# Performance work log

Hardware: AMD Instinct MI355X
Metric: run time of the kernel (lower is better)

The kernel has to match this reference:

```python
import jax, jax.numpy as jnp
import numpy as np

D = 64      # hidden_dim
H = 4       # num_attention_heads
DH = D // H # head_dim
B = 64      # graphs per batch
SCALE = np.float32(np.sqrt(DH))


def _sage(x, edge, wl, bl, wr):
    # SAGEConv: lin_l(mean_j x_j) + lin_r(x_i); mean over incoming edges (dst = edge[1])
    src, dst = edge[0], edge[1]
    n = x.shape[0]
    agg = jax.ops.segment_sum(x[src], dst, num_segments=n)
    cnt = jax.ops.segment_sum(jnp.ones((edge.shape[1],), x.dtype), dst, num_segments=n)
    mean = agg / jnp.maximum(cnt, 1.0)[:, None]
    return mean @ wl + bl + x @ wr


def _cross_attn(xq, xk, w, b):
    # w: [3, D, D] stacked (Q, K, V) projections; b: [3, D]
    Q = (xq @ w[0] + b[0]).reshape(-1, H, DH)  # [Nq, H, DH]
    K = (xk @ w[1] + b[1]).reshape(-1, H, DH)  # [Nk, H, DH]
    V = (xk @ w[2] + b[2]).reshape(-1, H, DH)
    scores = jnp.einsum('qhd,khd->hqk', Q, K) / SCALE  # [H, Nq, Nk]
    wgt = jax.nn.softmax(scores, axis=-1)
    out = jnp.einsum('hqk,khd->qhd', wgt, V)
    return out.reshape(xq.shape[0], D)


def _segment_mean(x, seg, num):
    s = jax.ops.segment_sum(x, seg, num_segments=num)
    c = jax.ops.segment_sum(jnp.ones((x.shape[0],), x.dtype), seg, num_segments=num)
    return s / jnp.maximum(c, 1.0)[:, None]


def setup_inputs() -> dict:
    key = jax.random.key(0)
    ks = jax.random.split(key, 32)
    N_MOL, N_PROT, E_MOL, E_PROT = 2048, 8192, 32768, 131072
    MOL_IN, PROT_IN = 32, 64

    def lin(k, i, o, s=None):
        s = 1.0 / np.sqrt(i) if s is None else s
        return (jax.random.normal(k, (i, o), jnp.float32) * s)

    inp = {
        'x_mol': jax.random.normal(ks[0], (N_MOL, MOL_IN), jnp.float32),
        'x_prot': jax.random.normal(ks[1], (N_PROT, PROT_IN), jnp.float32),
        'm1_wl': lin(ks[2], MOL_IN, D), 'm1_bl': jnp.zeros((D,), jnp.float32), 'm1_wr': lin(ks[3], MOL_IN, D),
        'm2_wl': lin(ks[4], D, D), 'm2_bl': jnp.zeros((D,), jnp.float32), 'm2_wr': lin(ks[5], D, D),
        'p1_wl': lin(ks[6], PROT_IN, D), 'p1_bl': jnp.zeros((D,), jnp.float32), 'p1_wr': lin(ks[7], PROT_IN, D),
        'p2_wl': lin(ks[8], D, D), 'p2_bl': jnp.zeros((D,), jnp.float32), 'p2_wr': lin(ks[9], D, D),
        'amp_w': jax.random.normal(ks[10], (3, D, D), jnp.float32) / np.sqrt(D),
        'amp_b': jnp.zeros((3, D), jnp.float32),
        'apm_w': jax.random.normal(ks[11], (3, D, D), jnp.float32) / np.sqrt(D),
        'apm_b': jnp.zeros((3, D), jnp.float32),
        'fc1_w': lin(ks[12], 2 * D, D), 'fc1_b': jnp.zeros((D,), jnp.float32),
        'fc2_w': lin(ks[13], D, 1), 'fc2_b': jnp.zeros((1,), jnp.float32),
        'edge_mol': jax.random.randint(ks[14], (2, E_MOL), 0, N_MOL, jnp.int32),
        'edge_prot': jax.random.randint(ks[15], (2, E_PROT), 0, N_PROT, jnp.int32),
        'batch_mol': jnp.sort(jax.random.randint(ks[16], (N_MOL,), 0, B, jnp.int32)),
        'batch_prot': jnp.sort(jax.random.randint(ks[17], (N_PROT,), 0, B, jnp.int32)),
    }
    return inp


def reference(x_mol, x_prot,
              m1_wl, m1_bl, m1_wr, m2_wl, m2_bl, m2_wr,
              p1_wl, p1_bl, p1_wr, p2_wl, p2_bl, p2_wr,
              amp_w, amp_b, apm_w, apm_b,
              fc1_w, fc1_b, fc2_w, fc2_b,
              edge_mol, edge_prot, batch_mol, batch_prot):
    # two SAGE conv blocks per graph, ReLU after each (HeteroConv with one edge type)
    h_mol = jax.nn.relu(_sage(x_mol, edge_mol, m1_wl, m1_bl, m1_wr))
    h_mol = jax.nn.relu(_sage(h_mol, edge_mol, m2_wl, m2_bl, m2_wr))
    h_prot = jax.nn.relu(_sage(x_prot, edge_prot, p1_wl, p1_bl, p1_wr))
    h_prot = jax.nn.relu(_sage(h_prot, edge_prot, p2_wl, p2_bl, p2_wr))
    # cross attention (mol queries prot, prot queries mol) + residual
    h_mol_c = h_mol + _cross_attn(h_mol, h_prot, amp_w, amp_b)
    h_prot_c = h_prot + _cross_attn(h_prot, h_mol, apm_w, apm_b)
    # global mean pool per graph
    z_mol = _segment_mean(h_mol_c, batch_mol, B)    # [B, D]
    z_prot = _segment_mean(h_prot_c, batch_prot, B)  # [B, D]
    z = jnp.concatenate([z_mol, z_prot], axis=1)     # [B, 2D]
    x = jax.nn.relu(z @ fc1_w + fc1_b)
    out = jax.nn.sigmoid(x @ fc2_w + fc2_b)
    return out.squeeze(-1)  # [B]
```

## Files before the change

kernel.cpp:

```cpp
#include <hip/hip_runtime.h>
#include <math.h>

#define D 64
#define NB 64

typedef __attribute__((ext_vector_type(8))) short bf16x8;
typedef __attribute__((ext_vector_type(4))) float f32x4;
typedef __attribute__((ext_vector_type(16))) float f32x16;

#define M3(a, b, c) fmaxf(fmaxf((a), (b)), (c))

__device__ __forceinline__ unsigned short f2bf(float f) {
    unsigned u = __float_as_uint(f);
    u += 0x7FFF + ((u >> 16) & 1);
    return (unsigned short)(u >> 16);
}
__device__ __forceinline__ unsigned pk_bf16(float lo, float hi) {
    unsigned r;
    asm("v_cvt_pk_bf16_f32 %0, %1, %2" : "=v"(r) : "v"(lo), "v"(hi));
    return r;
}
__device__ __forceinline__ float fexp2(float x) {
    float r;
    asm("v_exp_f32 %0, %1" : "=v"(r) : "v"(x));
    return r;
}

__global__ void k_zero(int* __restrict__ deg, int ndeg, float* __restrict__ zs, int nz) {
    int i = blockIdx.x * blockDim.x + threadIdx.x;
    if (i < ndeg) deg[i] = 0;
    if (i < nz) zs[i] = 0.f;
}

__global__ void k_hist2(const int* __restrict__ em, int Em,
                        const int* __restrict__ ep, int Ep,
                        int* __restrict__ degm, int* __restrict__ degp) {
    int i = blockIdx.x * blockDim.x + threadIdx.x;
    if (i < Em) atomicAdd(&degm[em[Em + i]], 1);
    int j = i - Em;
    if (j >= 0 && j < Ep) atomicAdd(&degp[ep[Ep + j]], 1);
}

__global__ __launch_bounds__(256) void k_scan2(
        const int* __restrict__ degm, int Nm, int* __restrict__ rpm, int* __restrict__ curm,
        const int* __restrict__ degp, int Np, int* __restrict__ rpp, int* __restrict__ curp) {
    __shared__ int sdeg[8192];
    __shared__ int chunk[256];
    const int* deg = blockIdx.x ? degp : degm;
    int N = blockIdx.x ? Np : Nm;
    int* rowptr = blockIdx.x ? rpp : rpm;
    int* cursor = blockIdx.x ? curp : curm;
    int t = threadIdx.x;
    for (int i = t; i < N; i += 256) sdeg[i] = deg[i];
    __syncthreads();
    int C = (N + 255) / 256;
    int start = t * C;
    int sum = 0;
    for (int i = 0; i < C; ++i)
        if (start + i < N) sum += sdeg[start + i];
    chunk[t] = sum;
    __syncthreads();
    for (int ofs = 1; ofs < 256; ofs <<= 1) {
        int v = (t >= ofs) ? chunk[t - ofs] : 0;
        __syncthreads();
        chunk[t] += v;
        __syncthreads();
    }
    int base = (t == 0) ? 0 : chunk[t - 1];
    for (int i = 0; i < C && start + i < N; ++i) {
        rowptr[start + i] = base;
        cursor[start + i] = base;
        base += sdeg[start + i];
    }
    if (t == 255) rowptr[N] = base;
}

__global__ void k_scatter2(const int* __restrict__ em, int Em, int* __restrict__ curm,
                           int* __restrict__ csrm,
                           const int* __restrict__ ep, int Ep, int* __restrict__ curp,
                           int* __restrict__ csrp) {
    int i = blockIdx.x * blockDim.x + threadIdx.x;
    if (i < Em) {
        int s = em[i], d = em[Em + i];
        csrm[atomicAdd(&curm[d], 1)] = s;
    }
    int j = i - Em;
    if (j >= 0 && j < Ep) {
        int s = ep[j], d = ep[Ep + j];
        csrp[atomicAdd(&curp[d], 1)] = s;
    }
}

template<int FIN>
__device__ __forceinline__ void gsage_body(
        const float* __restrict__ x, const int* __restrict__ rowptr,
        const int* __restrict__ csr, int N,
        const float* __restrict__ wl, const float* __restrict__ bl,
        const float* __restrict__ wr, float* __restrict__ out,
        int blk, float* __restrict__ swl, float* __restrict__ swr,
        float* __restrict__ sagg, float* __restrict__ sx) {
    for (int i = threadIdx.x; i < FIN * D; i += 256) { swl[i] = wl[i]; swr[i] = wr[i]; }
    int w = threadIdx.x >> 6;
    int lane = threadIdx.x & 63;
    int r = blk * 4 + w;
    if (r < N) {
        int e0 = rowptr[r], e1 = rowptr[r + 1];
        float inv = 1.0f / fmaxf((float)(e1 - e0), 1.0f);
        if (FIN == 64) {
            float a0 = 0.f, a1 = 0.f, a2 = 0.f, a3 = 0.f;
            int e = e0;
            for (; e + 3 < e1; e += 4) {
                a0 += x[(size_t)csr[e] * FIN + lane];
                a1 += x[(size_t)csr[e + 1] * FIN + lane];
                a2 += x[(size_t)csr[e + 2] * FIN + lane];
                a3 += x[(size_t)csr[e + 3] * FIN + lane];
            }
            for (; e < e1; ++e) a0 += x[(size_t)csr[e] * FIN + lane];
            sagg[w * 64 + lane] = ((a0 + a1) + (a2 + a3)) * inv;
            sx[w * 64 + lane] = x[(size_t)r * FIN + lane];
        } else {
            int f = lane & 31, half = lane >> 5;
            float a = 0.f;
            for (int e = e0 + half; e < e1; e += 2)
                a += x[(size_t)csr[e] * FIN + f];
            a += __shfl_xor(a, 32);
            if (half == 0) {
                sagg[w * 64 + f] = a * inv;
                sx[w * 64 + f] = x[(size_t)r * FIN + f];
            }
        }
    }
    __syncthreads();
    if (r >= N) return;
    int c = lane;
    float acc = bl[c];
    #pragma unroll 8
    for (int k = 0; k < FIN; ++k) {
        acc += sagg[w * 64 + k] * swl[k * D + c];
        acc += sx[w * 64 + k] * swr[k * D + c];
    }
    out[(size_t)r * D + c] = fmaxf(acc, 0.0f);
}

template<int FA, int FB>
__global__ __launch_bounds__(256) void k_gsage2(
        const float* __restrict__ xA, const int* __restrict__ rpA,
        const int* __restrict__ csrA, int NA,
        const float* __restrict__ wlA, const float* __restrict__ blA,
        const float* __restrict__ wrA, float* __restrict__ outA,
        const float* __restrict__ xB, const int* __restrict__ rpB,
        const int* __restrict__ csrB, int NB_,
        const float* __restrict__ wlB, const float* __restrict__ blB,
        const float* __restrict__ wrB, float* __restrict__ outB) {
    __shared__ float swl[64 * 64];
    __shared__ float swr[64 * 64];
    __shared__ float sagg[4 * 64];
    __shared__ float sx[4 * 64];
    int bA = NA / 4;
    if ((int)blockIdx.x < bA)
        gsage_body<FA>(xA, rpA, csrA, NA, wlA, blA, wrA, outA, blockIdx.x, swl, swr, sagg, sx);
    else
        gsage_body<FB>(xB, rpB, csrB, NB_, wlB, blB, wrB, outB, blockIdx.x - bA, swl, swr, sagg, sx);
}

__global__ __launch_bounds__(256) void k_qkv2(
        const float* __restrict__ xA, int NA, const float* __restrict__ xB, int NB_,
        const float* __restrict__ amp_w, const float* __restrict__ amp_b,
        const float* __restrict__ apm_w, const float* __restrict__ apm_b, float qs,
        unsigned short* __restrict__ QA, unsigned short* __restrict__ KA, unsigned short* __restrict__ VA,
        unsigned short* __restrict__ QB, unsigned short* __restrict__ KB, unsigned short* __restrict__ VB) {
    __shared__ float sq[D * D], sk[D * D], sv[D * D], sx[16 * D];
    int bA = NA / 16;
    const float *x, *wq, *bq, *wk, *bk, *wv, *bv;
    unsigned short *oq, *ok, *ov;
    int blk;
    if ((int)blockIdx.x < bA) {
        x = xA; blk = blockIdx.x;
        wq = amp_w;        bq = amp_b;
        wk = apm_w + 4096; bk = apm_b + 64;
        wv = apm_w + 8192; bv = apm_b + 128;
        oq = QA; ok = KA; ov = VA;
    } else {
        x = xB; blk = blockIdx.x - bA;
        wq = apm_w;        bq = apm_b;
        wk = amp_w + 4096; bk = amp_b + 64;
        wv = amp_w + 8192; bv = amp_b + 128;
        oq = QB; ok = KB; ov = VB;
    }
    for (int i = threadIdx.x; i < D * D; i += 256) { sq[i] = wq[i]; sk[i] = wk[i]; sv[i] = wv[i]; }
    int rbase = blk * 16;
    for (int i = threadIdx.x; i < 16 * D; i += 256) sx[i] = x[(size_t)rbase * D + i];
    __syncthreads();
    int c = threadIdx.x & 63;
    int r0 = (threadIdx.x >> 6) * 4;
    for (int rr = 0; rr < 4; ++rr) {
        int r = r0 + rr;
        float aq = bq[c], ak = bk[c], av = bv[c];
        #pragma unroll 8
        for (int k = 0; k < D; ++k) {
            float xv = sx[r * D + k];
            aq += xv * sq[k * D + c];
            ak += xv * sk[k * D + c];
            av += xv * sv[k * D + c];
        }
        size_t o = (size_t)(rbase + r) * D + c;
        oq[o] = f2bf(aq * qs);
        ok[o] = f2bf(ak);
        ov[o] = f2bf(av);
    }
}

__global__ void k_transp2(const unsigned short* __restrict__ inM, unsigned short* __restrict__ outM, int Nm,
                          const unsigned short* __restrict__ inP, unsigned short* __restrict__ outP, int Np) {
    __shared__ unsigned short tile[64][72];
    int bm = Nm >> 6;
    const unsigned short* in; unsigned short* out; int N;
    int blk = blockIdx.x;
    if (blk < bm) { in = inM; out = outM; N = Nm; }
    else { blk -= bm; in = inP; out = outP; N = Np; }
    int t = threadIdx.x;
    int rbase = blk * 64;
    {
        int r = t >> 2, c0 = (t & 3) * 16;
        const uint4* src = (const uint4*)(in + (size_t)(rbase + r) * 64 + c0);
        uint4 a = src[0], b = src[1];
        *(uint4*)(&tile[r][c0]) = a;
        *(uint4*)(&tile[r][c0 + 8]) = b;
    }
    __syncthreads();
    {
        int c = t >> 2, r0 = (t & 3) * 16;
        union { uint2 v2[4]; unsigned short s[16]; } u;
        #pragma unroll
        for (int i = 0; i < 16; ++i) u.s[i] = tile[r0 + i][c];
        int key0 = rbase + r0;
        int kc = key0 & ~31;
        int b16 = key0 & 16;
        unsigned short* op = out + (size_t)c * N;
        const int gmap[4] = {0, 8, 4, 12};
        #pragma unroll
        for (int b = 0; b < 4; ++b)
            *(uint2*)(op + kc + b16 + gmap[b]) = u.v2[b];
    }
    if (t < 8) {
        uint4 ones;
        ones.x = ones.y = ones.z = ones.w = 0x3F803F80u;
        *(uint4*)(out + (size_t)64 * N + rbase + t * 8) = ones;
    }
}

#define PVBLOCK(S, KB)                                                        \
    {                                                                         \
        float p[16];                                                          \
        _Pragma("unroll")                                                     \
        for (int i = 0; i < 16; ++i) p[i] = fexp2((S)[i]);                    \
        union { unsigned u[4]; bf16x8 v; } f1, f2;                            \
        f1.u[0] = pk_bf16(p[0], p[1]);   f1.u[1] = pk_bf16(p[2], p[3]);       \
        f1.u[2] = pk_bf16(p[4], p[5]);   f1.u[3] = pk_bf16(p[6], p[7]);       \
        f2.u[0] = pk_bf16(p[8], p[9]);   f2.u[1] = pk_bf16(p[10], p[11]);     \
        f2.u[2] = pk_bf16(p[12], p[13]); f2.u[3] = pk_bf16(p[14], p[15]);     \
        bf16x8 vb0 = *(const bf16x8*)(vbase + (KB) + half * 8);               \
        bf16x8 vb1 = *(const bf16x8*)(vbase + (KB) + 16 + half * 8);          \
        __builtin_amdgcn_s_setprio(1);                                        \
        o = __builtin_amdgcn_mfma_f32_32x32x16_bf16(f1.v, vb0, o, 0, 0, 0);   \
        o = __builtin_amdgcn_mfma_f32_32x32x16_bf16(f2.v, vb1, o, 0, 0, 0);   \
        __builtin_amdgcn_s_setprio(0);                                        \
    }

#define MAXTREE(cm, s0, s1)                                                   \
    {                                                                         \
        float c0 = M3(s0[0], s0[1], s0[2]);                                   \
        float c1 = M3(s0[3], s0[4], s0[5]);                                   \
        float c2 = M3(s0[6], s0[7], s0[8]);                                   \
        float c3 = M3(s0[9], s0[10], s0[11]);                                 \
        float c4 = M3(s0[12], s0[13], s0[14]);                                \
        float c5 = M3(s0[15], s1[0], s1[1]);                                  \
        float c6 = M3(s1[2], s1[3], s1[4]);                                   \
        float c7 = M3(s1[5], s1[6], s1[7]);                                   \
        float c8 = M3(s1[8], s1[9], s1[10]);                                  \
        float c9 = M3(s1[11], s1[12], s1[13]);                                \
        float ca = fmaxf(s1[14], s1[15]);                                     \
        float d0 = M3(c0, c1, c2);                                            \
        float d1 = M3(c3, c4, c5);                                            \
        float d2 = M3(c6, c7, c8);                                            \
        float d3 = M3(c9, ca, d0);                                            \
        cm = M3(d1, d2, d3);                                                  \
    }

__global__ __launch_bounds__(256) void k_attn2(
        const unsigned short* __restrict__ QmB, const unsigned short* __restrict__ KpB,
        const unsigned short* __restrict__ VpT, int Nm, int Np, int lsm,
        float* __restrict__ poM, float* __restrict__ pmM, float* __restrict__ plM,
        const unsigned short* __restrict__ QpB, const unsigned short* __restrict__ KmB,
        const unsigned short* __restrict__ VmT, int lsp,
        float* __restrict__ poP, float* __restrict__ pmP, float* __restrict__ plP) {
    const unsigned short *Q, *K, *Vt;
    int Nq, Nk, ls;
    float *po, *pm, *pl;
    if (blockIdx.y == 0) { Q = QmB; K = KpB; Vt = VpT; Nq = Nm; Nk = Np; ls = lsm; po = poM; pm = pmM; pl = plM; }
    else                 { Q = QpB; K = KmB; Vt = VmT; Nq = Np; Nk = Nm; ls = lsp; po = poP; pm = pmP; pl = plP; }
    int nqt = Nq >> 5;
    if ((int)blockIdx.x >= (nqt << ls)) return;
    const int qt = blockIdx.x >> ls;
    const int split = blockIdx.x & ((1 << ls) - 1);
    const int kchunk = Nk >> ls;
    const int h = threadIdx.x >> 6;
    const int lane = threadIdx.x & 63;
    const int cq = lane & 31;
    const int half = lane >> 5;
    const int h16 = h * 16;

    bf16x8 qb = *(const bf16x8*)(Q + ((size_t)(qt * 32 + cq) * D + h16 + half * 8));
    int drow = (cq < 16) ? (h16 + cq) : (cq == 16 ? 64 : h16 + 15);
    const unsigned short* vbase = Vt + (size_t)drow * Nk;

    f32x16 o, mC, zro;
    #pragma unroll
    for (int i = 0; i < 16; ++i) { o[i] = 0.f; zro[i] = 0.f; }
    float m;

    const int kstart = split * kchunk;
    {
        const int kb = kstart;
        bf16x8 ka0 = *(const bf16x8*)(K + ((size_t)(kb + cq) * D + h16 + half * 8));
        bf16x8 ka1 = *(const bf16x8*)(K + ((size_t)(kb + 32 + cq) * D + h16 + half * 8));
        f32x16 s0 = __builtin_amdgcn_mfma_f32_32x32x16_bf16(ka0, qb, zro, 0, 0, 0);
        f32x16 s1 = __builtin_amdgcn_mfma_f32_32x32x16_bf16(ka1, qb, zro, 0, 0, 0);
        float cm;
        MAXTREE(cm, s0, s1);
        #pragma unroll
        for (int off = 1; off < 64; off <<= 1) cm = fmaxf(cm, __shfl_xor(cm, off));
        m = cm;
        #pragma unroll
        for (int i = 0; i < 16; ++i) { s0[i] -= m; s1[i] -= m; mC[i] = -m; }
        PVBLOCK(s0, kb)
        PVBLOCK(s1, kb + 32)
    }
    for (int kb = kstart + 64; kb < kstart + kchunk; kb += 64) {
        bf16x8 ka0 = *(const bf16x8*)(K + ((size_t)(kb + cq) * D + h16 + half * 8));
        bf16x8 ka1 = *(const bf16x8*)(K + ((size_t)(kb + 32 + cq) * D + h16 + half * 8));
        f32x16 s0 = __builtin_amdgcn_mfma_f32_32x32x16_bf16(ka0, qb, mC, 0, 0, 0);
        f32x16 s1 = __builtin_amdgcn_mfma_f32_32x32x16_bf16(ka1, qb, mC, 0, 0, 0);
        float cm;
        MAXTREE(cm, s0, s1);
        if (__any(cm > 8.f)) {
            float cw = cm;
            #pragma unroll
            for (int off = 1; off < 64; off <<= 1) cw = fmaxf(cw, __shfl_xor(cw, off));
            float nm = fmaxf(m + cw, m);
            float sc = fexp2(m - nm);
            #pragma unroll
            for (int i = 0; i < 16; ++i) o[i] *= sc;
            float dl = nm - m;
            #pragma unroll
            for (int i = 0; i < 16; ++i) { s0[i] -= dl; s1[i] -= dl; mC[i] = -nm; }
            m = nm;
        }
        PVBLOCK(s0, kb)
        PVBLOCK(s1, kb + 32)
    }

    size_t pbase = (size_t)split * Nq + qt * 32;
    if (half == 0)
        pm[(pbase + cq) * 4 + h] = m;
    if (cq == 16) {
        #pragma unroll
        for (int r = 0; r < 16; ++r) {
            int qr = (r & 3) + 8 * (r >> 2) + 4 * half;
            pl[(pbase + qr) * 4 + h] = o[r];
        }
    }
    if (cq < 16) {
        #pragma unroll
        for (int r = 0; r < 16; ++r) {
            int qr = (r & 3) + 8 * (r >> 2) + 4 * half;
            po[(pbase + qr) * 64 + h16 + cq] = o[r];
        }
    }
}

template<int NS>
__device__ __forceinline__ void comb_body(
        const float* __restrict__ po, const float* __restrict__ pm,
        const float* __restrict__ pl, int Nq,
        const float* __restrict__ resid, const int* __restrict__ batch, int colOff,
        float* __restrict__ zsum, float* __restrict__ zcnt, int i) {
    int q = i >> 4;
    int part = i & 15;
    int d0 = part * 4;
    int h = part >> 2;
    float pmv[NS], plv[NS];
    #pragma unroll
    for (int s = 0; s < NS; ++s) pmv[s] = pm[((size_t)s * Nq + q) * 4 + h];
    #pragma unroll
    for (int s = 0; s < NS; ++s) plv[s] = pl[((size_t)s * Nq + q) * 4 + h];
    float M = pmv[0];
    #pragma unroll
    for (int s = 1; s < NS; ++s) M = fmaxf(M, pmv[s]);
    float4 O = {0.f, 0.f, 0.f, 0.f};
    float L = 0.f;
    #pragma unroll
    for (int s = 0; s < NS; ++s) {
        float wgt = fexp2(pmv[s] - M);
        float4 pv = *(const float4*)(po + ((size_t)s * Nq + q) * 64 + d0);
        O.x += pv.x * wgt; O.y += pv.y * wgt; O.z += pv.z * wgt; O.w += pv.w * wgt;
        L += plv[s] * wgt;
    }
    float invL = 1.0f / L;
    float4 rv = *(const float4*)(resid + (size_t)q * 64 + d0);
    int b = batch[q];
    float* zp = zsum + b * 128 + colOff + d0;
    atomicAdd(zp + 0, rv.x + O.x * invL);
    atomicAdd(zp + 1, rv.y + O.y * invL);
    atomicAdd(zp + 2, rv.z + O.z * invL);
    atomicAdd(zp + 3, rv.w + O.w * invL);
    if (part == 0) atomicAdd(&zcnt[b * 2 + (colOff ? 1 : 0)], 1.0f);
}

template<int NSM, int NSP>
__global__ void k_comb2t(
        const float* __restrict__ poM, const float* __restrict__ pmM, const float* __restrict__ plM,
        int Nm, const float* __restrict__ residM, const int* __restrict__ batchM,
        const float* __restrict__ poP, const float* __restrict__ pmP, const float* __restrict__ plP,
        int Np, const float* __restrict__ residP, const int* __restrict__ batchP,
        float* __restrict__ zsum, float* __restrict__ zcnt) {
    int idx = blockIdx.x * blockDim.x + threadIdx.x;
    int mtot = Nm * 16;
    if (idx < mtot)
        comb_body<NSM>(poM, pmM, plM, Nm, residM, batchM, 0, zsum, zcnt, idx);
    else if (idx - mtot < Np * 16)
        comb_body<NSP>(poP, pmP, plP, Np, residP, batchP, 64, zsum, zcnt, idx - mtot);
}

__global__ void k_comb2(
        const float* __restrict__ poM, const float* __restrict__ pmM, const float* __restrict__ plM,
        int nsM, int Nm, const float* __restrict__ residM, const int* __restrict__ batchM,
        const float* __restrict__ poP, const float* __restrict__ pmP, const float* __restrict__ plP,
        int nsP, int Np, const float* __restrict__ residP, const int* __restrict__ batchP,
        float* __restrict__ zsum, float* __restrict__ zcnt) {
    int idx = blockIdx.x * blockDim.x + threadIdx.x;
    const float *po, *pm, *pl, *resid;
    const int* batch;
    int ns, Nq, colOff, i;
    int mtot = Nm * 64;
    if (idx < mtot) {
        po = poM; pm = pmM; pl = plM; ns = nsM; Nq = Nm; resid = residM; batch = batchM; colOff = 0; i = idx;
    } else {
        i = idx - mtot;
        if (i >= Np * 64) return;
        po = poP; pm = pmP; pl = plP; ns = nsP; Nq = Np; resid = residP; batch = batchP; colOff = 64;
    }
    int q = i >> 6, d = i & 63, h = d >> 4;
    float M = -1e30f;
    for (int s = 0; s < ns; ++s)
        M = fmaxf(M, pm[((size_t)s * Nq + q) * 4 + h]);
    float O = 0.f, L = 0.f;
    for (int s = 0; s < ns; ++s) {
        float wgt = fexp2(pm[((size_t)s * Nq + q) * 4 + h] - M);
        O += po[((size_t)s * Nq + q) * 64 + d] * wgt;
        L += pl[((size_t)s * Nq + q) * 4 + h] * wgt;
    }
    float val = resid[i] + O / L;
    int b = batch[q];
    atomicAdd(&zsum[b * 128 + colOff + d], val);
    if (d == 0) atomicAdd(&zcnt[b * 2 + (colOff ? 1 : 0)], 1.0f);
}

__global__ __launch_bounds__(256) void k_head2(
        const float* __restrict__ zsum, const float* __restrict__ zcnt,
        const float* __restrict__ fc1w, const float* __restrict__ fc1b,
        const float* __restrict__ fc2w, const float* __restrict__ fc2b,
        float* __restrict__ out) {
    int b = blockIdx.x * 4 + (threadIdx.x >> 6);
    int c = threadIdx.x & 63;
    float inv0 = 1.0f / fmaxf(zcnt[b * 2 + 0], 1.0f);
    float inv1 = 1.0f / fmaxf(zcnt[b * 2 + 1], 1.0f);
    float acc = fc1b[c];
    #pragma unroll 8
    for (int k = 0; k < 128; ++k) {
        float zv = zsum[b * 128 + k] * (k < 64 ? inv0 : inv1);
        acc += zv * fc1w[k * 64 + c];
    }
    float v = fmaxf(acc, 0.0f) * fc2w[c];
    #pragma unroll
    for (int off = 32; off > 0; off >>= 1) v += __shfl_xor(v, off);
    if (c == 0) out[b] = 1.0f / (1.0f + __expf(-(v + fc2b[0])));
}

extern "C" void kernel_launch(void* const* d_in, const int* in_sizes, int n_in,
                              void* d_out, int out_size, void* d_ws, size_t ws_size,
                              hipStream_t stream) {
    const float* x_mol  = (const float*)d_in[0];
    const float* x_prot = (const float*)d_in[1];
    const float* m1_wl = (const float*)d_in[2];
    const float* m1_bl = (const float*)d_in[3];
    const float* m1_wr = (const float*)d_in[4];
    const float* m2_wl = (const float*)d_in[5];
    const float* m2_bl = (const float*)d_in[6];
    const float* m2_wr = (const float*)d_in[7];
    const float* p1_wl = (const float*)d_in[8];
    const float* p1_bl = (const float*)d_in[9];
    const float* p1_wr = (const float*)d_in[10];
    const float* p2_wl = (const float*)d_in[11];
    const float* p2_bl = (const float*)d_in[12];
    const float* p2_wr = (const float*)d_in[13];
    const float* amp_w = (const float*)d_in[14];
    const float* amp_b = (const float*)d_in[15];
    const float* apm_w = (const float*)d_in[16];
    const float* apm_b = (const float*)d_in[17];
    const float* fc1_w = (const float*)d_in[18];
    const float* fc1_b = (const float*)d_in[19];
    const float* fc2_w = (const float*)d_in[20];
    const float* fc2_b = (const float*)d_in[21];
    const int* edge_mol  = (const int*)d_in[22];
    const int* edge_prot = (const int*)d_in[23];
    const int* batch_mol  = (const int*)d_in[24];
    const int* batch_prot = (const int*)d_in[25];
    float* out = (float*)d_out;

    const int N_MOL  = in_sizes[0] / 32;
    const int N_PROT = in_sizes[1] / 64;
    const int E_MOL  = in_sizes[22] / 2;
    const int E_PROT = in_sizes[23] / 2;

    char* base = (char*)d_ws;
    size_t off = 0;
    auto alloc = [&](size_t bytes) -> void* {
        void* p = base + off;
        off = (off + bytes + 255) & ~(size_t)255;
        return p;
    };
    float* h_mol1   = (float*)alloc((size_t)N_MOL * D * sizeof(float));
    float* h_mol2   = (float*)alloc((size_t)N_MOL * D * sizeof(float));
    float* h_prot1  = (float*)alloc((size_t)N_PROT * D * sizeof(float));
    float* h_prot2  = (float*)alloc((size_t)N_PROT * D * sizeof(float));
    float* zsum     = (float*)alloc((NB * 128 + NB * 2) * sizeof(float));
    float* zcnt     = zsum + NB * 128;
    unsigned short* Qm_b = (unsigned short*)alloc((size_t)N_MOL * D * 2);
    unsigned short* Km_b = (unsigned short*)alloc((size_t)N_MOL * D * 2);
    unsigned short* Vm_b = (unsigned short*)alloc((size_t)N_MOL * D * 2);
    unsigned short* Vm_t = (unsigned short*)alloc((size_t)N_MOL * (D + 1) * 2);
    unsigned short* Qp_b = (unsigned short*)alloc((size_t)N_PROT * D * 2);
    unsigned short* Kp_b = (unsigned short*)alloc((size_t)N_PROT * D * 2);
    unsigned short* Vp_b = (unsigned short*)alloc((size_t)N_PROT * D * 2);
    unsigned short* Vp_t = (unsigned short*)alloc((size_t)N_PROT * (D + 1) * 2);
    int* deg      = (int*)alloc(((size_t)N_MOL + N_PROT) * sizeof(int));
    int* deg_m    = deg;
    int* deg_p    = deg + N_MOL;
    int* rp_m     = (int*)alloc(((size_t)N_MOL + 1) * sizeof(int));
    int* cur_m    = (int*)alloc((size_t)N_MOL * sizeof(int));
    int* csr_m    = (int*)alloc((size_t)E_MOL * sizeof(int));
    int* rp_p     = (int*)alloc(((size_t)N_PROT + 1) * sizeof(int));
    int* cur_p    = (int*)alloc((size_t)N_PROT * sizeof(int));
    int* csr_p    = (int*)alloc((size_t)E_PROT * sizeof(int));

    int nsm = 16; while (nsm > 1 && (N_PROT % (64 * nsm))) nsm >>= 1;
    int nsp = 4;  while (nsp > 1 && (N_MOL % (64 * nsp)))  nsp >>= 1;
    int lsm = 31 - __builtin_clz(nsm);
    int lsp = 31 - __builtin_clz(nsp);
    float* poM = (float*)alloc((size_t)nsm * N_MOL * 64 * sizeof(float));
    float* pmM = (float*)alloc((size_t)nsm * N_MOL * 4 * sizeof(float));
    float* plM = (float*)alloc((size_t)nsm * N_MOL * 4 * sizeof(float));
    float* poP = (float*)alloc((size_t)nsp * N_PROT * 64 * sizeof(float));
    float* pmP = (float*)alloc((size_t)nsp * N_PROT * 4 * sizeof(float));
    float* plP = (float*)alloc((size_t)nsp * N_PROT * 4 * sizeof(float));

    const int BLK = 256;
    dim3 blk(BLK);
    const float QS = 0.25f * 1.4426950408889634f;

    {
        int ndeg = N_MOL + N_PROT;
        int nz = NB * 128 + NB * 2;
        int mx = ndeg > nz ? ndeg : nz;
        k_zero<<<(mx + BLK - 1) / BLK, blk, 0, stream>>>(deg, ndeg, zsum, nz);
    }
    int Etot = E_MOL + E_PROT;
    k_hist2<<<(Etot + BLK - 1) / BLK, blk, 0, stream>>>(edge_mol, E_MOL, edge_prot, E_PROT, deg_m, deg_p);
    k_scan2<<<2, blk, 0, stream>>>(deg_m, N_MOL, rp_m, cur_m, deg_p, N_PROT, rp_p, cur_p);
    k_scatter2<<<(Etot + BLK - 1) / BLK, blk, 0, stream>>>(edge_mol, E_MOL, cur_m, csr_m,
                                                           edge_prot, E_PROT, cur_p, csr_p);

    k_gsage2<32, 64><<<N_MOL / 4 + N_PROT / 4, blk, 0, stream>>>(
        x_mol,  rp_m, csr_m, N_MOL,  m1_wl, m1_bl, m1_wr, h_mol1,
        x_prot, rp_p, csr_p, N_PROT, p1_wl, p1_bl, p1_wr, h_prot1);
    k_gsage2<64, 64><<<N_MOL / 4 + N_PROT / 4, blk, 0, stream>>>(
        h_mol1,  rp_m, csr_m, N_MOL,  m2_wl, m2_bl, m2_wr, h_mol2,
        h_prot1, rp_p, csr_p, N_PROT, p2_wl, p2_bl, p2_wr, h_prot2);

    k_qkv2<<<N_MOL / 16 + N_PROT / 16, blk, 0, stream>>>(
        h_mol2, N_MOL, h_prot2, N_PROT, amp_w, amp_b, apm_w, apm_b, QS,
        Qm_b, Km_b, Vm_b, Qp_b, Kp_b, Vp_b);

    k_transp2<<<N_MOL / 64 + N_PROT / 64, blk, 0, stream>>>(Vm_b, Vm_t, N_MOL, Vp_b, Vp_t, N_PROT);

    int gxm = (N_MOL / 32) * nsm;
    int gxp = (N_PROT / 32) * nsp;
    int gx = gxm > gxp ? gxm : gxp;
    k_attn2<<<dim3(gx, 2), blk, 0, stream>>>(
        Qm_b, Kp_b, Vp_t, N_MOL, N_PROT, lsm, poM, pmM, plM,
        Qp_b, Km_b, Vm_t, lsp, poP, pmP, plP);

    if (nsm == 16 && nsp == 4) {
        int tot = (N_MOL + N_PROT) * 16;
        k_comb2t<16, 4><<<(tot + BLK - 1) / BLK, blk, 0, stream>>>(
            poM, pmM, plM, N_MOL, h_mol2, batch_mol,
            poP, pmP, plP, N_PROT, h_prot2, batch_prot,
            zsum, zcnt);
    } else {
        k_comb2<<<((N_MOL + N_PROT) * 64 + BLK - 1) / BLK, blk, 0, stream>>>(
            poM, pmM, plM, nsm, N_MOL, h_mol2, batch_mol,
            poP, pmP, plP, nsp, N_PROT, h_prot2, batch_prot,
            zsum, zcnt);
    }

    k_head2<<<16, blk, 0, stream>>>(zsum, zcnt, fc1_w, fc1_b, fc2_w, fc2_b, out);
}
```

Measured before the change: 209.6 us.

## Replace atomic mean-pool with segment-start deterministic pooling kernel

Instead of scattering float atomics into per-graph sums from the combine kernel, the combine now writes the residual-added attention output to a buffer. A separate pooling kernel then reduces each graph's contiguous node range, using segment starts computed from the batch arrays, which assumes the batch indices are sorted. The zero-init kernel becomes a memset. This targets the contention from many atomics on 64x128 pool cells, at the cost of an extra full write and read of node features plus two extra launches.

```diff
diff --git a/kernel.cpp b/kernel.cpp
--- a/kernel.cpp
+++ b/kernel.cpp
@@ -24,12 +24,6 @@
     float r;
     asm("v_exp_f32 %0, %1" : "=v"(r) : "v"(x));
     return r;
-}
-
-__global__ void k_zero(int* __restrict__ deg, int ndeg, float* __restrict__ zs, int nz) {
-    int i = blockIdx.x * blockDim.x + threadIdx.x;
-    if (i < ndeg) deg[i] = 0;
-    if (i < nz) zs[i] = 0.f;
 }
 
 __global__ void k_hist2(const int* __restrict__ em, int Em,
@@ -88,6 +82,26 @@
     if (j >= 0 && j < Ep) {
         int s = ep[j], d = ep[Ep + j];
         csrp[atomicAdd(&curp[d], 1)] = s;
+    }
+}
+
+__global__ void k_bstart2(const int* __restrict__ bm, int Nm, int* __restrict__ bsM,
+                          const int* __restrict__ bp, int Np, int* __restrict__ bsP) {
+    int i = blockIdx.x * blockDim.x + threadIdx.x;
+    if (i < Nm) {
+        int cur = bm[i];
+        int prev = (i == 0) ? -1 : bm[i - 1];
+        for (int b = prev + 1; b <= cur; ++b) bsM[b] = i;
+        if (i == Nm - 1)
+            for (int b = cur + 1; b <= NB; ++b) bsM[b] = Nm;
+    }
+    int j = i - Nm;
+    if (j >= 0 && j < Np) {
+        int cur = bp[j];
+        int prev = (j == 0) ? -1 : bp[j - 1];
+        for (int b = prev + 1; b <= cur; ++b) bsP[b] = j;
+        if (j == Np - 1)
+            for (int b = cur + 1; b <= NB; ++b) bsP[b] = Np;
     }
 }
 
@@ -383,8 +397,7 @@
 __device__ __forceinline__ void comb_body(
         const float* __restrict__ po, const float* __restrict__ pm,
         const float* __restrict__ pl, int Nq,
-        const float* __restrict__ resid, const int* __restrict__ batch, int colOff,
-        float* __restrict__ zsum, float* __restrict__ zcnt, int i) {
+        const float* __restrict__ resid, float* __restrict__ outc, int i) {
     int q = i >> 4;
     int part = i & 15;
     int d0 = part * 4;
@@ -408,47 +421,44 @@
     }
     float invL = 1.0f / L;
     float4 rv = *(const float4*)(resid + (size_t)q * 64 + d0);
-    int b = batch[q];
-    float* zp = zsum + b * 128 + colOff + d0;
-    atomicAdd(zp + 0, rv.x + O.x * invL);
-    atomicAdd(zp + 1, rv.y + O.y * invL);
-    atomicAdd(zp + 2, rv.z + O.z * invL);
-    atomicAdd(zp + 3, rv.w + O.w * invL);
-    if (part == 0) atomicAdd(&zcnt[b * 2 + (colOff ? 1 : 0)], 1.0f);
+    float4 res;
+    res.x = rv.x + O.x * invL;
+    res.y = rv.y + O.y * invL;
+    res.z = rv.z + O.z * invL;
+    res.w = rv.w + O.w * invL;
+    *(float4*)(outc + (size_t)q * 64 + d0) = res;
 }
 
 template<int NSM, int NSP>
 __global__ void k_comb2t(
         const float* __restrict__ poM, const float* __restrict__ pmM, const float* __restrict__ plM,
-        int Nm, const float* __restrict__ residM, const int* __restrict__ batchM,
+        int Nm, const float* __restrict__ residM, float* __restrict__ outM,
         const float* __restrict__ poP, const float* __restrict__ pmP, const float* __restrict__ plP,
-        int Np, const float* __restrict__ residP, const int* __restrict__ batchP,
-        float* __restrict__ zsum, float* __restrict__ zcnt) {
+        int Np, const float* __restrict__ residP, float* __restrict__ outP) {
     int idx = blockIdx.x * blockDim.x + threadIdx.x;
     int mtot = Nm * 16;
     if (idx < mtot)
-        comb_body<NSM>(poM, pmM, plM, Nm, residM, batchM, 0, zsum, zcnt, idx);
+        comb_body<NSM>(poM, pmM, plM, Nm, residM, outM, idx);
     else if (idx - mtot < Np * 16)
-        comb_body<NSP>(poP, pmP, plP, Np, residP, batchP, 64, zsum, zcnt, idx - mtot);
+        comb_body<NSP>(poP, pmP, plP, Np, residP, outP, idx - mtot);
 }
 
 __global__ void k_comb2(
         const float* __restrict__ poM, const float* __restrict__ pmM, const float* __restrict__ plM,
-        int nsM, int Nm, const float* __restrict__ residM, const int* __restrict__ batchM,
+        int nsM, int Nm, const float* __restrict__ residM, float* __restrict__ outM,
         const float* __restrict__ poP, const float* __restrict__ pmP, const float* __restrict__ plP,
-        int nsP, int Np, const float* __restrict__ residP, const int* __restrict__ batchP,
-        float* __restrict__ zsum, float* __restrict__ zcnt) {
+        int nsP, int Np, const float* __restrict__ residP, float* __restrict__ outP) {
     int idx = blockIdx.x * blockDim.x + threadIdx.x;
     const float *po, *pm, *pl, *resid;
-    const int* batch;
-    int ns, Nq, colOff, i;
+    float* outc;
+    int ns, Nq, i;
     int mtot = Nm * 64;
     if (idx < mtot) {
-        po = poM; pm = pmM; pl = plM; ns = nsM; Nq = Nm; resid = residM; batch = batchM; colOff = 0; i = idx;
+        po = poM; pm = pmM; pl = plM; ns = nsM; Nq = Nm; resid = residM; outc = outM; i = idx;
     } else {
         i = idx - mtot;
         if (i >= Np * 64) return;
-        po = poP; pm = pmP; pl = plP; ns = nsP; Nq = Np; resid = residP; batch = batchP; colOff = 64;
+        po = poP; pm = pmP; pl = plP; ns = nsP; Nq = Np; resid = residP; outc = outP;
     }
     int q = i >> 6, d = i & 63, h = d >> 4;
     float M = -1e30f;
@@ -460,10 +470,31 @@
         O += po[((size_t)s * Nq + q) * 64 + d] * wgt;
         L += pl[((size_t)s * Nq + q) * 4 + h] * wgt;
     }
-    float val = resid[i] + O / L;
-    int b = batch[q];
-    atomicAdd(&zsum[b * 128 + colOff + d], val);
-    if (d == 0) atomicAdd(&zcnt[b * 2 + (colOff ? 1 : 0)], 1.0f);
+    outc[i] = resid[i] + O / L;
+}
+
+__global__ __launch_bounds__(256) void k_pool2(
+        const float* __restrict__ hM, const int* __restrict__ bsM,
+        const float* __restrict__ hP, const int* __restrict__ bsP,
+        float* __restrict__ zsum, float* __restrict__ zcnt) {
+    __shared__ float red[4][64];
+    int b = blockIdx.x & 63;
+    int isP = blockIdx.x >> 6;
+    const float* h = isP ? hP : hM;
+    const int* bs = isP ? bsP : bsM;
+    int colOff = isP ? 64 : 0;
+    int n0 = bs[b], n1 = bs[b + 1];
+    int w = threadIdx.x >> 6, c = threadIdx.x & 63;
+    float acc = 0.f;
+    for (int n = n0 + w; n < n1; n += 4)
+        acc += h[(size_t)n * 64 + c];
+    red[w][c] = acc;
+    __syncthreads();
+    if (w == 0) {
+        float s = (red[0][c] + red[1][c]) + (red[2][c] + red[3][c]);
+        zsum[b * 128 + colOff + c] = s;
+        if (c == 0) zcnt[b * 2 + isP] = (float)(n1 - n0);
+    }
 }
 
 __global__ __launch_bounds__(256) void k_head2(
@@ -534,6 +565,8 @@
     float* h_mol2   = (float*)alloc((size_t)N_MOL * D * sizeof(float));
     float* h_prot1  = (float*)alloc((size_t)N_PROT * D * sizeof(float));
     float* h_prot2  = (float*)alloc((size_t)N_PROT * D * sizeof(float));
+    float* h_mol_c  = (float*)alloc((size_t)N_MOL * D * sizeof(float));
+    float* h_prot_c = (float*)alloc((size_t)N_PROT * D * sizeof(float));
     float* zsum     = (float*)alloc((NB * 128 + NB * 2) * sizeof(float));
     float* zcnt     = zsum + NB * 128;
     unsigned short* Qm_b = (unsigned short*)alloc((size_t)N_MOL * D * 2);
@@ -553,6 +586,8 @@
     int* rp_p     = (int*)alloc(((size_t)N_PROT + 1) * sizeof(int));
     int* cur_p    = (int*)alloc((size_t)N_PROT * sizeof(int));
     int* csr_p    = (int*)alloc((size_t)E_PROT * sizeof(int));
+    int* bsM      = (int*)alloc((NB + 1) * sizeof(int));
+    int* bsP      = (int*)alloc((NB + 1) * sizeof(int));
 
     int nsm = 16; while (nsm > 1 && (N_PROT % (64 * nsm))) nsm >>= 1;
     int nsp = 4;  while (nsp > 1 && (N_MOL % (64 * nsp)))  nsp >>= 1;
@@ -569,14 +604,11 @@
     dim3 blk(BLK);
     const float QS = 0.25f * 1.4426950408889634f;
 
-    {
-        int ndeg = N_MOL + N_PROT;
-        int nz = NB * 128 + NB * 2;
-        int mx = ndeg > nz ? ndeg : nz;
-        k_zero<<<(mx + BLK - 1) / BLK, blk, 0, stream>>>(deg, ndeg, zsum, nz);
-    }
+    hipMemsetAsync(deg, 0, ((size_t)N_MOL + N_PROT) * sizeof(int), stream);
     int Etot = E_MOL + E_PROT;
     k_hist2<<<(Etot + BLK - 1) / BLK, blk, 0, stream>>>(edge_mol, E_MOL, edge_prot, E_PROT, deg_m, deg_p);
+    k_bstart2<<<(N_MOL + N_PROT + BLK - 1) / BLK, blk, 0, stream>>>(
+        batch_mol, N_MOL, bsM, batch_prot, N_PROT, bsP);
     k_scan2<<<2, blk, 0, stream>>>(deg_m, N_MOL, rp_m, cur_m, deg_p, N_PROT, rp_p, cur_p);
     k_scatter2<<<(Etot + BLK - 1) / BLK, blk, 0, stream>>>(edge_mol, E_MOL, cur_m, csr_m,
                                                            edge_prot, E_PROT, cur_p, csr_p);
@@ -604,15 +636,15 @@
     if (nsm == 16 && nsp == 4) {
         int tot = (N_MOL + N_PROT) * 16;
         k_comb2t<16, 4><<<(tot + BLK - 1) / BLK, blk, 0, stream>>>(
-            poM, pmM, plM, N_MOL, h_mol2, batch_mol,
-            poP, pmP, plP, N_PROT, h_prot2, batch_prot,
-            zsum, zcnt);
+            poM, pmM, plM, N_MOL, h_mol2, h_mol_c,
+            poP, pmP, plP, N_PROT, h_prot2, h_prot_c);
     } else {
         k_comb2<<<((N_MOL + N_PROT) * 64 + BLK - 1) / BLK, blk, 0, stream>>>(
-            poM, pmM, plM, nsm, N_MOL, h_mol2, batch_mol,
-            poP, pmP, plP, nsp, N_PROT, h_prot2, batch_prot,
-            zsum, zcnt);
-    }
+            poM, pmM, plM, nsm, N_MOL, h_mol2, h_mol_c,
+            poP, pmP, plP, nsp, N_PROT, h_prot2, h_prot_c);
+    }
+
+    k_pool2<<<128, blk, 0, stream>>>(h_mol_c, bsM, h_prot_c, bsP, zsum, zcnt);
 
     k_head2<<<16, blk, 0, stream>>>(zsum, zcnt, fc1_w, fc1_b, fc2_w, fc2_b, out);
 }
```

Measured after the change: 175.2 us. -16.4%, faster.
